# Performance work log

Hardware: AMD Instinct MI355X
Metric: run time of the kernel (lower is better)

Reference implementation:

```python
import jax, jax.numpy as jnp
import numpy as np

B, S, D, E = 4, 4096, 2048, 64
NOISE_STD = 1.0


def setup_inputs() -> dict:
    key = jax.random.key(0)
    k1, k2, k3, k4 = jax.random.split(key, 4)
    x = jax.random.normal(k1, (B, S, D), dtype=jnp.float32)
    lim = float(np.sqrt(6.0 / (D + E)))  # glorot_uniform
    W_gate = jax.random.uniform(k2, (D, E), jnp.float32, -lim, lim)
    # keras inits noise_dense kernel to zeros; use tiny random values so the
    # noise path is numerically exercised (zeros would make it trivially ln(2)).
    W_noise = 0.02 * jax.random.normal(k3, (D, E), dtype=jnp.float32)
    noise = jax.random.normal(k4, (B * S, E), dtype=jnp.float32)
    return {"x": x, "W_gate": W_gate, "W_noise": W_noise, "noise": noise, "top_k": 2}


def reference(x, W_gate, W_noise, noise, top_k):
    b, s, d = x.shape
    e = W_gate.shape[1]
    xf = x.reshape(-1, d)                         # [N, D], N = b*s
    gate_logits = xf @ W_gate                     # [N, E]
    # training-mode noise injection
    noise_logits = xf @ W_noise                   # [N, E]
    nstd = jax.nn.softplus(noise_logits) * (NOISE_STD / (e * e))
    gate_logits = gate_logits + noise * nstd
    # top-k mask + masked softmax
    top_vals, top_idx = jax.lax.top_k(gate_logits, top_k)   # [N, K]
    n = gate_logits.shape[0]
    mask = jnp.zeros_like(gate_logits).at[jnp.arange(n)[:, None], top_idx].set(1.0)
    masked_logits = jnp.where(mask > 0, gate_logits, jnp.float32(-1e9))
    expert_weights = jax.nn.softmax(masked_logits, axis=-1)  # [N, E]
    raw_gate_probs = jax.nn.softmax(gate_logits, axis=-1)    # [N, E]
    expert_weights = expert_weights.reshape(b, s, e)
    expert_indices = top_idx.reshape(b, s, top_k).astype(jnp.int32)
    return expert_weights, expert_indices, gate_logits, raw_gate_probs
```

## Files before the change

### kernel.cpp

```cpp
#include <hip/hip_runtime.h>
#include <math.h>


typedef _Float16 f16;
typedef f16  f16x8  __attribute__((ext_vector_type(8)));
typedef float f32x16 __attribute__((ext_vector_type(16)));

constexpr int NROWS = 16384;
constexpr int DDIM  = 2048;
constexpr int NE    = 64;
constexpr int BM    = 32;
constexpr int KI    = 32;
constexpr int NITER = 1024 / KI;
constexpr float NSCALE = 1.0f / 4096.0f;

__device__ __forceinline__ int a_off(int buf, int h, int s, int j4) {
    return (((buf * 2 + h) * 2 + s) * 2 + j4) * 1024;
}

__device__ __forceinline__ float softplus_f(float x) {
    return fmaxf(x, 0.0f) + log1pf(expf(-fabsf(x)));
}

__device__ __forceinline__ void gload_lds16(const void* g, void* l) {
    __builtin_amdgcn_global_load_lds(
        (const __attribute__((address_space(1))) void*)g,
        (__attribute__((address_space(3))) void*)l, 16, 0, 0);
}

#define PIPE_BAR(N) do {                                                   \
    asm volatile("s_waitcnt vmcnt(" #N ") lgkmcnt(0)" ::: "memory");       \
    __builtin_amdgcn_sched_barrier(0);                                     \
    __builtin_amdgcn_s_barrier();                                          \
    __builtin_amdgcn_sched_barrier(0);                                     \
} while (0)

__global__ __launch_bounds__(256) void wprep_kernel(
    const float* __restrict__ Wg, const float* __restrict__ Wn,
    f16* __restrict__ ws)
{
    int t = blockIdx.x * 256 + threadIdx.x;
    int S = t >> 8;
    int f = (t >> 6) & 3;
    int l = t & 63;
    int k0  = S * 16 + (l >> 5) * 8;
    int col = f * 32 + (l & 31);
    const float* src = (col < NE) ? (Wg + col) : (Wn + col - NE);
    f16x8 hp, lp;
    #pragma unroll
    for (int j = 0; j < 8; ++j) {
        float w  = src[(size_t)(k0 + j) * NE];
        f16 h    = (f16)w;
        float hf = (float)h;
        hp[j] = h;
        lp[j] = (f16)((w - hf) * 64.0f);
    }
    size_t base = (size_t)(S * 4 + f) * 1024;
    *(f16x8*)(ws + base + l * 8)       = hp;
    *(f16x8*)(ws + base + 512 + l * 8) = lp;
}

__global__ __launch_bounds__(512, 4) void gemm_gating(
    const float* __restrict__ x, const f16* __restrict__ wfrag,
    const float* __restrict__ noise,
    float* __restrict__ out_w, float* __restrict__ out_idx,
    float* __restrict__ out_logits, float* __restrict__ out_probs)
{
    __shared__ __align__(16) char smem[49152];
    const int tid = threadIdx.x;
    const int l   = tid & 63;
    const int w   = tid >> 6;
    const int h   = w >> 2;
    const int f   = w & 3;
    const int row0 = blockIdx.x * BM;

    f32x16 acc1, acc2;
    #pragma unroll
    for (int r = 0; r < 16; ++r) { acc1[r] = 0.0f; acc2[r] = 0.0f; }

    const int h_s  = w >> 2, s_s = (w >> 1) & 1, j4_s = w & 1;
    const float* aSrc = x + (size_t)(row0 + (l & 31)) * DDIM
                          + h_s * 1024 + s_s * 16 + (l >> 5) * 8 + j4_s * 4;
    auto stageA = [&](int t, int buf) {
        gload_lds16(aSrc + (size_t)t * KI, smem + a_off(buf, h_s, s_s, j4_s));
    };

    const f16* bBase = wfrag + (size_t)f * 1024 + l * 8;
    f16x8 bh0c, bl0c, bh1c, bl1c;
    f16x8 bh0n, bl0n, bh1n, bl1n;
    auto loadB = [&](int t, f16x8& H0, f16x8& L0, f16x8& H1, f16x8& L1) {
        const f16* p = bBase + (size_t)(h * 64 + t * 2) * 4096;
        H0 = *(const f16x8*)p;
        L0 = *(const f16x8*)(p + 512);
        H1 = *(const f16x8*)(p + 4096);
        L1 = *(const f16x8*)(p + 4096 + 512);
    };

    auto compute = [&](int buf) {
        #pragma unroll
        for (int s = 0; s < 2; ++s) {
            float4 a0 = *(const float4*)(smem + a_off(buf, h, s, 0) + l * 16);
            float4 a1 = *(const float4*)(smem + a_off(buf, h, s, 1) + l * 16);
            float xs[8] = {a0.x, a0.y, a0.z, a0.w, a1.x, a1.y, a1.z, a1.w};
            f16x8 Ah, Al;
            #pragma unroll
            for (int j = 0; j < 8; ++j) {
                f16 hh   = (f16)xs[j];
                float hf = (float)hh;
                Ah[j] = hh;
                Al[j] = (f16)((xs[j] - hf) * 64.0f);
            }
            f16x8 Bh = s ? bh1c : bh0c;
            f16x8 Bl = s ? bl1c : bl0c;
            acc1 = __builtin_amdgcn_mfma_f32_32x32x16_f16(Ah, Bh, acc1, 0, 0, 0);
            acc2 = __builtin_amdgcn_mfma_f32_32x32x16_f16(Ah, Bl, acc2, 0, 0, 0);
            acc2 = __builtin_amdgcn_mfma_f32_32x32x16_f16(Al, Bh, acc2, 0, 0, 0);
        }
    };

    stageA(0, 0);
    loadB(0, bh0c, bl0c, bh1c, bl1c);
    stageA(1, 1);
    stageA(2, 2);

    loadB(1, bh0n, bl0n, bh1n, bl1n);
    stageA(3, 3);
    PIPE_BAR(7);
    compute(0);
    bh0c = bh0n; bl0c = bl0n; bh1c = bh1n; bl1c = bl1n;

    for (int t = 1; t < NITER - 3; ++t) {
        loadB(t + 1, bh0n, bl0n, bh1n, bl1n);
        stageA(t + 3, (t + 3) & 3);
        PIPE_BAR(6);
        compute(t & 3);
        bh0c = bh0n; bl0c = bl0n; bh1c = bh1n; bl1c = bl1n;
    }
    {
        int t = NITER - 3;
        loadB(t + 1, bh0n, bl0n, bh1n, bl1n);
        PIPE_BAR(5);
        compute(t & 3);
        bh0c = bh0n; bl0c = bl0n; bh1c = bh1n; bl1c = bl1n;
    }
    {
        int t = NITER - 2;
        loadB(t + 1, bh0n, bl0n, bh1n, bl1n);
        PIPE_BAR(4);
        compute(t & 3);
        bh0c = bh0n; bl0c = bl0n; bh1c = bh1n; bl1c = bl1n;
    }
    PIPE_BAR(0);
    compute((NITER - 1) & 3);
    __syncthreads();

    float* mg  = (float*)(smem + 32768);
    if (h == 1) {
        #pragma unroll
        for (int r = 0; r < 16; ++r) {
            float cv = fmaf(acc2[r], 0.015625f, acc1[r]);
            int row = (r & 3) + 8 * (r >> 2) + 4 * (l >> 5);
            int col = f * 32 + (l & 31);
            mg[row * 128 + col] = cv;
        }
    }
    __syncthreads();

    float* lgf = (float*)smem;
    if (h == 0) {
        #pragma unroll
        for (int r = 0; r < 16; ++r) {
            float cv = fmaf(acc2[r], 0.015625f, acc1[r]);
            int row = (r & 3) + 8 * (r >> 2) + 4 * (l >> 5);
            int col = f * 32 + (l & 31);
            lgf[row * 132 + col] = cv + mg[row * 128 + col];
        }
    }
    __syncthreads();

    {
        const int pr = tid & 31;
        const int c4 = tid >> 5;
        const int n1 = row0 + pr;
        float4 G  = *(const float4*)(lgf + pr * 132 + c4 * 4);
        float4 NL = *(const float4*)(lgf + pr * 132 + 64 + c4 * 4);
        float4 NZ = *(const float4*)(noise + (size_t)n1 * NE + c4 * 4);
        G.x += NZ.x * softplus_f(NL.x) * NSCALE;
        G.y += NZ.y * softplus_f(NL.y) * NSCALE;
        G.z += NZ.z * softplus_f(NL.z) * NSCALE;
        G.w += NZ.w * softplus_f(NL.w) * NSCALE;
        *(float4*)(lgf + pr * 132 + c4 * 4) = G;
        *(float4*)(out_logits + (size_t)n1 * NE + c4 * 4) = G;
    }
    __syncthreads();

    if (w < 4) {
        const int g2   = l >> 3;
        const int c    = l & 7;
        const int row2 = w * 8 + g2;
        const int n2   = row0 + row2;

        float mv[8];
        {
            const float4* mr = (const float4*)(lgf + row2 * 132 + c * 8);
            float4 m0 = mr[0], m1 = mr[1];
            mv[0]=m0.x; mv[1]=m0.y; mv[2]=m0.z; mv[3]=m0.w;
            mv[4]=m1.x; mv[5]=m1.y; mv[6]=m1.z; mv[7]=m1.w;
        }
        float v0 = -INFINITY, v1 = -INFINITY;
        int i0 = 0, i1 = 0;
        #pragma unroll
        for (int j = 0; j < 8; ++j) {
            float v = mv[j]; int e = c * 8 + j;
            if (v > v0) { v1 = v0; i1 = i0; v0 = v; i0 = e; }
            else if (v > v1) { v1 = v; i1 = e; }
        }
        #pragma unroll
        for (int m = 1; m <= 4; m <<= 1) {
            float ov0 = __shfl_xor(v0, m), ov1 = __shfl_xor(v1, m);
            int   oi0 = __shfl_xor(i0, m), oi1 = __shfl_xor(i1, m);
            if (ov0 > v0) {
                bool keep = (v0 > ov1);
                v1 = keep ? v0 : ov1; i1 = keep ? i0 : oi1;
                v0 = ov0; i0 = oi0;
            } else if (ov0 > v1) {
                v1 = ov0; i1 = oi0;
            }
        }
        const int srcl = l & 56;
        v0 = __shfl(v0, srcl); i0 = __shfl(i0, srcl);
        v1 = __shfl(v1, srcl); i1 = __shfl(i1, srcl);

        float se = 0.0f;
        #pragma unroll
        for (int j = 0; j < 8; ++j) se += expf(mv[j] - v0);
        se += __shfl_xor(se, 1); se += __shfl_xor(se, 2); se += __shfl_xor(se, 4);
        float inv_se = 1.0f / se;

        float t  = expf(v1 - v0);
        float w0 = 1.0f / (1.0f + t);
        float w1 = t * w0;

        float pr[8], wt[8];
        #pragma unroll
        for (int j = 0; j < 8; ++j) {
            int e = c * 8 + j;
            pr[j] = expf(mv[j] - v0) * inv_se;
            wt[j] = (e == i0) ? w0 : ((e == i1) ? w1 : 0.0f);
        }
        *(float4*)(out_probs + (size_t)n2 * NE + c * 8)     = make_float4(pr[0], pr[1], pr[2], pr[3]);
        *(float4*)(out_probs + (size_t)n2 * NE + c * 8 + 4) = make_float4(pr[4], pr[5], pr[6], pr[7]);
        *(float4*)(out_w + (size_t)n2 * NE + c * 8)         = make_float4(wt[0], wt[1], wt[2], wt[3]);
        *(float4*)(out_w + (size_t)n2 * NE + c * 8 + 4)     = make_float4(wt[4], wt[5], wt[6], wt[7]);
        if (c == 0) {
            *(float2*)(out_idx + (size_t)n2 * 2) = make_float2((float)i0, (float)i1);
        }
    }
}

extern "C" void kernel_launch(void* const* d_in, const int* in_sizes, int n_in,
                              void* d_out, int out_size, void* d_ws, size_t ws_size,
                              hipStream_t stream) {
    (void)in_sizes; (void)n_in; (void)ws_size; (void)out_size;
    const float* x     = (const float*)d_in[0];
    const float* Wg    = (const float*)d_in[1];
    const float* Wn    = (const float*)d_in[2];
    const float* noise = (const float*)d_in[3];
    float* out        = (float*)d_out;
    float* out_w      = out;
    float* out_idx    = out + (size_t)NROWS * NE;
    float* out_logits = out_idx + (size_t)NROWS * 2;
    float* out_probs  = out_logits + (size_t)NROWS * NE;
    f16* wfrag = (f16*)d_ws;

    wprep_kernel<<<128, 256, 0, stream>>>(Wg, Wn, wfrag);
    gemm_gating<<<NROWS / BM, 512, 0, stream>>>(
        x, wfrag, noise, out_w, out_idx, out_logits, out_probs);
}
```

Baseline: 56.98 us.

## Convert A tile to fp16 hi/lo once in registers before LDS staging

Replaces the direct global-to-LDS async loads of fp32 x tiles with register loads kept several iterations ahead. Each thread splits its own elements into fp16 hi/lo and writes them to LDS, so the split is done once per element instead of redundantly by each consumer wave. The MFMA loop now reads ready fp16 fragments from LDS. The cost is extra VGPRs for in-flight float4 prefetches and a software pipeline whose global-load waits are left to the compiler instead of explicit vmcnt control.

```diff
diff --git a/kernel.cpp b/kernel.cpp
--- a/kernel.cpp
+++ b/kernel.cpp
@@ -3,6 +3,7 @@
 
 
 typedef _Float16 f16;
+typedef f16  f16x4  __attribute__((ext_vector_type(4)));
 typedef f16  f16x8  __attribute__((ext_vector_type(8)));
 typedef float f32x16 __attribute__((ext_vector_type(16)));
 
@@ -14,26 +15,20 @@
 constexpr int NITER = 1024 / KI;
 constexpr float NSCALE = 1.0f / 4096.0f;
 
-__device__ __forceinline__ int a_off(int buf, int h, int s, int j4) {
-    return (((buf * 2 + h) * 2 + s) * 2 + j4) * 1024;
+__device__ __forceinline__ int a_off(int buf, int h, int s, int v) {
+    return (((buf * 2 + h) * 2 + s) * 2 + v) * 1024;
 }
 
 __device__ __forceinline__ float softplus_f(float x) {
     return fmaxf(x, 0.0f) + log1pf(expf(-fabsf(x)));
 }
 
-__device__ __forceinline__ void gload_lds16(const void* g, void* l) {
-    __builtin_amdgcn_global_load_lds(
-        (const __attribute__((address_space(1))) void*)g,
-        (__attribute__((address_space(3))) void*)l, 16, 0, 0);
-}
-
-#define PIPE_BAR(N) do {                                                   \
-    asm volatile("s_waitcnt vmcnt(" #N ") lgkmcnt(0)" ::: "memory");       \
-    __builtin_amdgcn_sched_barrier(0);                                     \
-    __builtin_amdgcn_s_barrier();                                          \
-    __builtin_amdgcn_sched_barrier(0);                                     \
-} while (0)
+__device__ __forceinline__ void tile_bar() {
+    asm volatile("s_waitcnt lgkmcnt(0)" ::: "memory");
+    __builtin_amdgcn_sched_barrier(0);
+    __builtin_amdgcn_s_barrier();
+    __builtin_amdgcn_sched_barrier(0);
+}
 
 __global__ __launch_bounds__(256) void wprep_kernel(
     const float* __restrict__ Wg, const float* __restrict__ Wn,
@@ -78,16 +73,29 @@
     #pragma unroll
     for (int r = 0; r < 16; ++r) { acc1[r] = 0.0f; acc2[r] = 0.0f; }
 
-    const int h_s  = w >> 2, s_s = (w >> 1) & 1, j4_s = w & 1;
+    const int h_s = w >> 2, s_s = (w >> 1) & 1, j4 = w & 1;
     const float* aSrc = x + (size_t)(row0 + (l & 31)) * DDIM
-                          + h_s * 1024 + s_s * 16 + (l >> 5) * 8 + j4_s * 4;
-    auto stageA = [&](int t, int buf) {
-        gload_lds16(aSrc + (size_t)t * KI, smem + a_off(buf, h_s, s_s, j4_s));
+                          + h_s * 1024 + s_s * 16 + (l >> 5) * 8 + j4 * 4;
+    auto loadA = [&](int t) -> float4 {
+        return *(const float4*)(aSrc + (size_t)t * KI);
+    };
+    auto cvtWrite = [&](float4 xv, int tt) {
+        int buf = tt & 3;
+        float xs[4] = {xv.x, xv.y, xv.z, xv.w};
+        f16x4 hi, lo;
+        #pragma unroll
+        for (int j = 0; j < 4; ++j) {
+            f16 hh   = (f16)xs[j];
+            float hf = (float)hh;
+            hi[j] = hh;
+            lo[j] = (f16)((xs[j] - hf) * 64.0f);
+        }
+        *(f16x4*)(smem + a_off(buf, h_s, s_s, 0) + l * 16 + j4 * 8) = hi;
+        *(f16x4*)(smem + a_off(buf, h_s, s_s, 1) + l * 16 + j4 * 8) = lo;
     };
 
     const f16* bBase = wfrag + (size_t)f * 1024 + l * 8;
-    f16x8 bh0c, bl0c, bh1c, bl1c;
-    f16x8 bh0n, bl0n, bh1n, bl1n;
+    f16x8 bh0c, bl0c, bh1c, bl1c, bh0n, bl0n, bh1n, bl1n;
     auto loadB = [&](int t, f16x8& H0, f16x8& L0, f16x8& H1, f16x8& L1) {
         const f16* p = bBase + (size_t)(h * 64 + t * 2) * 4096;
         H0 = *(const f16x8*)p;
@@ -96,20 +104,12 @@
         L1 = *(const f16x8*)(p + 4096 + 512);
     };
 
-    auto compute = [&](int buf) {
+    auto compute = [&](int t) {
+        int buf = t & 3;
         #pragma unroll
         for (int s = 0; s < 2; ++s) {
-            float4 a0 = *(const float4*)(smem + a_off(buf, h, s, 0) + l * 16);
-            float4 a1 = *(const float4*)(smem + a_off(buf, h, s, 1) + l * 16);
-            float xs[8] = {a0.x, a0.y, a0.z, a0.w, a1.x, a1.y, a1.z, a1.w};
-            f16x8 Ah, Al;
-            #pragma unroll
-            for (int j = 0; j < 8; ++j) {
-                f16 hh   = (f16)xs[j];
-                float hf = (float)hh;
-                Ah[j] = hh;
-                Al[j] = (f16)((xs[j] - hf) * 64.0f);
-            }
+            f16x8 Ah = *(const f16x8*)(smem + a_off(buf, h, s, 0) + l * 16);
+            f16x8 Al = *(const f16x8*)(smem + a_off(buf, h, s, 1) + l * 16);
             f16x8 Bh = s ? bh1c : bh0c;
             f16x8 Bl = s ? bl1c : bl0c;
             acc1 = __builtin_amdgcn_mfma_f32_32x32x16_f16(Ah, Bh, acc1, 0, 0, 0);
@@ -118,40 +118,24 @@
         }
     };
 
-    stageA(0, 0);
+    float4 r0 = loadA(0);
+    float4 r1 = loadA(1);
     loadB(0, bh0c, bl0c, bh1c, bl1c);
-    stageA(1, 1);
-    stageA(2, 2);
-
-    loadB(1, bh0n, bl0n, bh1n, bl1n);
-    stageA(3, 3);
-    PIPE_BAR(7);
-    compute(0);
-    bh0c = bh0n; bl0c = bl0n; bh1c = bh1n; bl1c = bl1n;
-
-    for (int t = 1; t < NITER - 3; ++t) {
-        loadB(t + 1, bh0n, bl0n, bh1n, bl1n);
-        stageA(t + 3, (t + 3) & 3);
-        PIPE_BAR(6);
-        compute(t & 3);
+    float4 sc = loadA(2);
+    float4 sm = loadA(3);
+    cvtWrite(r0, 0);
+    cvtWrite(r1, 1);
+
+    for (int t = 0; t < NITER; ++t) {
+        tile_bar();
+        float4 sn = sc;
+        if (t + 4 < NITER) sn = loadA(t + 4);
+        if (t + 1 < NITER) loadB(t + 1, bh0n, bl0n, bh1n, bl1n);
+        if (t + 2 < NITER) cvtWrite(sc, t + 2);
+        compute(t);
+        sc = sm; sm = sn;
         bh0c = bh0n; bl0c = bl0n; bh1c = bh1n; bl1c = bl1n;
     }
-    {
-        int t = NITER - 3;
-        loadB(t + 1, bh0n, bl0n, bh1n, bl1n);
-        PIPE_BAR(5);
-        compute(t & 3);
-        bh0c = bh0n; bl0c = bl0n; bh1c = bh1n; bl1c = bl1n;
-    }
-    {
-        int t = NITER - 2;
-        loadB(t + 1, bh0n, bl0n, bh1n, bl1n);
-        PIPE_BAR(4);
-        compute(t & 3);
-        bh0c = bh0n; bl0c = bl0n; bh1c = bh1n; bl1c = bl1n;
-    }
-    PIPE_BAR(0);
-    compute((NITER - 1) & 3);
     __syncthreads();
 
     float* mg  = (float*)(smem + 32768);
```

Result: no change. 56.08 us (-1.6%).

## Swizzle A tile LDS layout and triple-buffer B fragments in registers

Applied to the files above, without the earlier changes.

Changes how x rows are staged into LDS: each wave now DMA-loads 8 rows at a time in a row-major layout with an XOR swizzle on the 16-byte column chunks. Compute reads back through the same swizzle, which is meant to cut LDS bank conflicts and make the global loads more contiguous. The B fragment prefetch becomes a three-slot register rotation, unrolled by 3, in place of the copy-based double buffer. This lets B loads run one iteration further ahead, and the vmcnt wait thresholds are retuned to match. The risk is higher register pressure and fragile hand-counted vmcnt values near the tail, where DMA issues are skipped.

```diff
diff --git a/kernel.cpp b/kernel.cpp
--- a/kernel.cpp
+++ b/kernel.cpp
@@ -14,8 +14,8 @@
 constexpr int NITER = 1024 / KI;
 constexpr float NSCALE = 1.0f / 4096.0f;
 
-__device__ __forceinline__ int a_off(int buf, int h, int s, int j4) {
-    return (((buf * 2 + h) * 2 + s) * 2 + j4) * 1024;
+__device__ __forceinline__ int a_base(int buf, int h) {
+    return (buf * 2 + h) * 4096;
 }
 
 __device__ __forceinline__ float softplus_f(float x) {
@@ -78,29 +78,33 @@
     #pragma unroll
     for (int r = 0; r < 16; ++r) { acc1[r] = 0.0f; acc2[r] = 0.0f; }
 
-    const int h_s  = w >> 2, s_s = (w >> 1) & 1, j4_s = w & 1;
-    const float* aSrc = x + (size_t)(row0 + (l & 31)) * DDIM
-                          + h_s * 1024 + s_s * 16 + (l >> 5) * 8 + j4_s * 4;
-    auto stageA = [&](int t, int buf) {
-        gload_lds16(aSrc + (size_t)t * KI, smem + a_off(buf, h_s, s_s, j4_s));
+    const int hs = w >> 2, rg = w & 3;
+    const int sr = rg * 8 + (l >> 3);
+    const int sc = (l & 7) ^ (l >> 3);
+    const float* aSrc = x + (size_t)(row0 + sr) * DDIM + hs * 1024 + sc * 4;
+    char* aDst = smem;
+    auto dmaA = [&](int t) {
+        gload_lds16(aSrc + (size_t)t * KI,
+                    aDst + a_base((t) & 3, hs) + rg * 1024 + l * 16);
     };
 
     const f16* bBase = wfrag + (size_t)f * 1024 + l * 8;
-    f16x8 bh0c, bl0c, bh1c, bl1c;
-    f16x8 bh0n, bl0n, bh1n, bl1n;
-    auto loadB = [&](int t, f16x8& H0, f16x8& L0, f16x8& H1, f16x8& L1) {
-        const f16* p = bBase + (size_t)(h * 64 + t * 2) * 4096;
-        H0 = *(const f16x8*)p;
-        L0 = *(const f16x8*)(p + 512);
-        H1 = *(const f16x8*)(p + 4096);
-        L1 = *(const f16x8*)(p + 4096 + 512);
-    };
-
-    auto compute = [&](int buf) {
+#define LOADB(t, H0, L0, H1, L1) do {                                       \
+        const f16* _p = bBase + (size_t)(h * 64 + (t) * 2) * 4096;          \
+        H0 = *(const f16x8*)_p;          L0 = *(const f16x8*)(_p + 512);    \
+        H1 = *(const f16x8*)(_p + 4096); L1 = *(const f16x8*)(_p + 4608);   \
+    } while (0)
+
+    const int R   = l & 31;
+    const int swz = R & 7;
+    auto compute = [&](int t, const f16x8& Bh0, const f16x8& Bl0,
+                              const f16x8& Bh1, const f16x8& Bl1) {
+        const char* tile = smem + a_base(t & 3, h) + R * 128;
         #pragma unroll
         for (int s = 0; s < 2; ++s) {
-            float4 a0 = *(const float4*)(smem + a_off(buf, h, s, 0) + l * 16);
-            float4 a1 = *(const float4*)(smem + a_off(buf, h, s, 1) + l * 16);
+            int g0 = s * 4 + (l >> 5) * 2;
+            float4 a0 = *(const float4*)(tile + ((g0 ^ swz) * 16));
+            float4 a1 = *(const float4*)(tile + (((g0 + 1) ^ swz) * 16));
             float xs[8] = {a0.x, a0.y, a0.z, a0.w, a1.x, a1.y, a1.z, a1.w};
             f16x8 Ah, Al;
             #pragma unroll
@@ -110,49 +114,44 @@
                 Ah[j] = hh;
                 Al[j] = (f16)((xs[j] - hf) * 64.0f);
             }
-            f16x8 Bh = s ? bh1c : bh0c;
-            f16x8 Bl = s ? bl1c : bl0c;
+            const f16x8& Bh = s ? Bh1 : Bh0;
+            const f16x8& Bl = s ? Bl1 : Bl0;
             acc1 = __builtin_amdgcn_mfma_f32_32x32x16_f16(Ah, Bh, acc1, 0, 0, 0);
             acc2 = __builtin_amdgcn_mfma_f32_32x32x16_f16(Ah, Bl, acc2, 0, 0, 0);
             acc2 = __builtin_amdgcn_mfma_f32_32x32x16_f16(Al, Bh, acc2, 0, 0, 0);
         }
     };
 
-    stageA(0, 0);
-    loadB(0, bh0c, bl0c, bh1c, bl1c);
-    stageA(1, 1);
-    stageA(2, 2);
-
-    loadB(1, bh0n, bl0n, bh1n, bl1n);
-    stageA(3, 3);
-    PIPE_BAR(7);
-    compute(0);
-    bh0c = bh0n; bl0c = bl0n; bh1c = bh1n; bl1c = bl1n;
-
-    for (int t = 1; t < NITER - 3; ++t) {
-        loadB(t + 1, bh0n, bl0n, bh1n, bl1n);
-        stageA(t + 3, (t + 3) & 3);
-        PIPE_BAR(6);
-        compute(t & 3);
-        bh0c = bh0n; bl0c = bl0n; bh1c = bh1n; bl1c = bl1n;
-    }
-    {
-        int t = NITER - 3;
-        loadB(t + 1, bh0n, bl0n, bh1n, bl1n);
-        PIPE_BAR(5);
-        compute(t & 3);
-        bh0c = bh0n; bl0c = bl0n; bh1c = bh1n; bl1c = bl1n;
-    }
-    {
-        int t = NITER - 2;
-        loadB(t + 1, bh0n, bl0n, bh1n, bl1n);
-        PIPE_BAR(4);
-        compute(t & 3);
-        bh0c = bh0n; bl0c = bl0n; bh1c = bh1n; bl1c = bl1n;
-    }
-    PIPE_BAR(0);
-    compute((NITER - 1) & 3);
-    __syncthreads();
+    f16x8 s0a, s0b, s0c, s0d;
+    f16x8 s1a, s1b, s1c, s1d;
+    f16x8 s2a, s2b, s2c, s2d;
+
+    dmaA(0); dmaA(1); dmaA(2);
+    LOADB(0, s0a, s0b, s0c, s0d);
+    LOADB(1, s1a, s1b, s1c, s1d);
+
+    for (int t = 0; t < 30; t += 3) {
+        PIPE_BAR(10);
+        if (t + 3 < NITER) dmaA(t + 3);
+        LOADB(t + 2, s2a, s2b, s2c, s2d);
+        compute(t, s0a, s0b, s0c, s0d);
+
+        PIPE_BAR(10);
+        if (t + 4 < NITER) dmaA(t + 4);
+        LOADB(t + 3, s0a, s0b, s0c, s0d);
+        compute(t + 1, s1a, s1b, s1c, s1d);
+
+        PIPE_BAR(10);
+        if (t + 5 < NITER) dmaA(t + 5);
+        LOADB(t + 4, s1a, s1b, s1c, s1d);
+        compute(t + 2, s2a, s2b, s2c, s2d);
+    }
+    PIPE_BAR(9);
+    compute(30, s0a, s0b, s0c, s0d);
+    PIPE_BAR(4);
+    compute(31, s1a, s1b, s1c, s1d);
+    __syncthreads();
+#undef LOADB
 
     float* mg  = (float*)(smem + 32768);
     if (h == 1) {
```

After: 56.35 us. Within noise of the previous version (-1.1%).
